# Optimization experiments

Measured on AMD Instinct MI355X. Metric: run time of the kernel, lower is better.

## Reference

```python
import jax, jax.numpy as jnp
import numpy as np

B, S, E, H = 2, 2048, 512, 8
HD = E // H  # head dim = 64


def setup_inputs() -> dict:
    key = jax.random.key(0)
    k1, k2, k3 = jax.random.split(key, 3)
    scale_qkv = (6.0 / (E + 3 * E)) ** 0.5  # xavier-uniform-like scale
    scale_o = (6.0 / (E + E)) ** 0.5
    return {
        "X": jax.random.normal(k1, (B, S, E), dtype=jnp.float32),
        "Wqkv": jax.random.uniform(k2, (E, 3 * E), jnp.float32, -scale_qkv, scale_qkv),
        "bqkv": jnp.zeros((3 * E,), jnp.float32),
        "Wo": jax.random.uniform(k3, (E, E), jnp.float32, -scale_o, scale_o),
        "bo": jnp.zeros((E,), jnp.float32),
    }


def reference(X, Wqkv, bqkv, Wo, bo):
    b, s, e = X.shape
    # qkv projection: [B,S,3E] -> [B,S,H,3*HD] -> [B,H,S,3*HD]
    qkv = X @ Wqkv + bqkv
    qkv = qkv.reshape(b, s, H, 3 * HD).transpose(0, 2, 1, 3)
    q, k, v = jnp.array_split(qkv, 3, axis=-1)  # each [B,H,S,HD]
    # naive scaled dot-product attention (full score matrix, per source)
    attn_logits = jnp.einsum("bhqd,bhkd->bhqk", q, k) / jnp.sqrt(jnp.float32(HD))
    attention = jax.nn.softmax(attn_logits, axis=-1)  # [B,H,S,S]
    values = jnp.einsum("bhqk,bhkd->bhqd", attention, v)
    values = values.transpose(0, 2, 1, 3).reshape(b, s, e)
    o = values @ Wo + bo
    return (o, attention)
```

## Files before the change

### kernel.cpp

```cpp
#include <hip/hip_runtime.h>

typedef unsigned short u16;
typedef u16 u16x2 __attribute__((ext_vector_type(2)));
typedef u16 u16x4 __attribute__((ext_vector_type(4)));
typedef u16 u16x8 __attribute__((ext_vector_type(8)));
typedef __bf16 bf16x8 __attribute__((ext_vector_type(8)));
typedef float f32x4 __attribute__((ext_vector_type(4)));
typedef float f32x2 __attribute__((ext_vector_type(2)));

#define MFMA16(A, B, C) __builtin_amdgcn_mfma_f32_16x16x32_bf16(A, B, C, 0, 0, 0)

#define SB 2
#define SS 2048
#define SE 512
#define SH 8
#define SHD 64

__device__ __forceinline__ u16 f2b(float f) {
  union { float f; unsigned u; } v;
  v.f = f;
  unsigned r = v.u + 0x7FFFu + ((v.u >> 16) & 1u);
  return (u16)(r >> 16);
}

__device__ __forceinline__ bf16x8 as_bf16x8(u16x8 v) {
  return __builtin_bit_cast(bf16x8, v);
}

__global__ __launch_bounds__(256)
void convx_kernel(const float* __restrict__ X, u16* __restrict__ Xb)
{
  const int i = (blockIdx.x * 256 + threadIdx.x) * 4;
  const float4 v = *(const float4*)&X[i];
  u16x4 o;
  o[0] = f2b(v.x); o[1] = f2b(v.y); o[2] = f2b(v.z); o[3] = f2b(v.w);
  *(u16x4*)&Xb[i] = o;
}

__global__ __launch_bounds__(256)
void wtrans_kernel(const float* __restrict__ in, u16* __restrict__ out, int N)
{
  __shared__ float t[32][33];
  const int tid = threadIdx.x;
  const int r = tid >> 3, c4 = (tid & 7) * 4;
  const int k0 = blockIdx.y * 32, n0 = blockIdx.x * 32;
  const float4 v = *(const float4*)&in[(size_t)(k0 + r) * N + n0 + c4];
  t[r][c4 + 0] = v.x; t[r][c4 + 1] = v.y; t[r][c4 + 2] = v.z; t[r][c4 + 3] = v.w;
  __syncthreads();
  u16x4 o;
  o[0] = f2b(t[c4 + 0][r]);
  o[1] = f2b(t[c4 + 1][r]);
  o[2] = f2b(t[c4 + 2][r]);
  o[3] = f2b(t[c4 + 3][r]);
  *(u16x4*)&out[(n0 + r) * 512 + k0 + c4] = o;
}

template <int MODE>
__global__ __launch_bounds__(256, 2)
void gemm_kernel(const u16* __restrict__ A, const u16* __restrict__ Bt,
                 const float* __restrict__ bias,
                 u16* __restrict__ Q, u16* __restrict__ K, u16* __restrict__ Vt,
                 float* __restrict__ Out)
{
  __shared__ __align__(16) u16 As[128 * 40];
  __shared__ __align__(16) u16 Bs[128 * 40];
  const int tid  = threadIdx.x;
  const int lane = tid & 63, wave = tid >> 6, quad = lane >> 4, l16 = lane & 15;
  const int m0 = blockIdx.y * 128, n0 = blockIdx.x * 128;
  const int wr = (wave >> 1) * 64, wc = (wave & 1) * 64;
  const int sr = tid >> 2, sc = (tid & 3) * 8;

  const f32x4 z4 = {0.f, 0.f, 0.f, 0.f};
  f32x4 acc[4][4];
#pragma unroll
  for (int i = 0; i < 4; i++)
#pragma unroll
    for (int j = 0; j < 4; j++) acc[i][j] = z4;

  for (int k0 = 0; k0 < 512; k0 += 32) {
    const u16x8 a0 = *(const u16x8*)&A[(m0 + sr) * 512 + k0 + sc];
    const u16x8 a1 = *(const u16x8*)&A[(m0 + 64 + sr) * 512 + k0 + sc];
    const u16x8 b0 = *(const u16x8*)&Bt[(n0 + sr) * 512 + k0 + sc];
    const u16x8 b1 = *(const u16x8*)&Bt[(n0 + 64 + sr) * 512 + k0 + sc];
    __syncthreads();
    *(u16x8*)&As[sr * 40 + sc]        = a0;
    *(u16x8*)&As[(64 + sr) * 40 + sc] = a1;
    *(u16x8*)&Bs[sr * 40 + sc]        = b0;
    *(u16x8*)&Bs[(64 + sr) * 40 + sc] = b1;
    __syncthreads();
    bf16x8 af[4], bf[4];
#pragma unroll
    for (int i = 0; i < 4; i++) {
      af[i] = as_bf16x8(*(const u16x8*)&As[(wr + i * 16 + l16) * 40 + quad * 8]);
      bf[i] = as_bf16x8(*(const u16x8*)&Bs[(wc + i * 16 + l16) * 40 + quad * 8]);
    }
#pragma unroll
    for (int i = 0; i < 4; i++)
#pragma unroll
      for (int j = 0; j < 4; j++) acc[i][j] = MFMA16(af[i], bf[j], acc[i][j]);
  }

#pragma unroll
  for (int tm = 0; tm < 4; tm++) {
#pragma unroll
    for (int tn = 0; tn < 4; tn++) {
#pragma unroll
      for (int r = 0; r < 4; r++) {
        const int gm = m0 + wr + tm * 16 + quad * 4 + r;
        const int gn = n0 + wc + tn * 16 + l16;
        const float v = acc[tm][tn][r] + bias[gn];
        if (MODE == 0) {
          const int bb = gm >> 11, s = gm & 2047;
          const int hh = gn / 192, j = gn - hh * 192;
          const int bh = bb * SH + hh;
          if (j < 64)
            Q[(bh * SS + s) * SHD + j] = f2b(v * 0.125f);
          else if (j < 128)
            K[(bh * SS + s) * SHD + (j - 64)] = f2b(v);
          else
            Vt[(bh * SHD + (j - 128)) * SS + s] = f2b(v);
        } else {
          Out[gm * 512 + gn] = v;
        }
      }
    }
  }
}

#define PSTR 264
#define PWAVE (16 * PSTR)

__global__ __launch_bounds__(512, 4)
void attn_kernel(const u16* __restrict__ Q, const u16* __restrict__ K,
                 const u16* __restrict__ Vt, u16* __restrict__ values,
                 float* __restrict__ attn)
{
  __shared__ __align__(16) u16 p_lds[8 * PWAVE];
  __shared__ float srm[8][16];
  __shared__ float srl[8][16];

  const int tid  = threadIdx.x;
  const int lane = tid & 63, wave = tid >> 6, quad = lane >> 4, l16 = lane & 15;
  const int q0 = blockIdx.x * 16;
  const int h = blockIdx.y, b = blockIdx.z, bh = b * SH + h;

  const u16* Qb = Q + (size_t)bh * SS * SHD;
  const u16* Kb = K + (size_t)bh * SS * SHD;
  const u16* Vb = Vt + (size_t)bh * SHD * SS;

  const bf16x8 aq0 = as_bf16x8(*(const u16x8*)&Qb[(q0 + l16) * SHD + quad * 8]);
  const bf16x8 aq1 = as_bf16x8(*(const u16x8*)&Qb[(q0 + l16) * SHD + 32 + quad * 8]);

  f32x4 acc[16];
#pragma unroll
  for (int ct = 0; ct < 16; ct++) {
    const int kb = wave * 256 + ct * 16;
    bf16x8 bk0 = as_bf16x8(*(const u16x8*)&Kb[(kb + l16) * SHD + quad * 8]);
    bf16x8 bk1 = as_bf16x8(*(const u16x8*)&Kb[(kb + l16) * SHD + 32 + quad * 8]);
    f32x4 c = {0.f, 0.f, 0.f, 0.f};
    c = MFMA16(aq0, bk0, c);
    c = MFMA16(aq1, bk1, c);
    acc[ct] = c;
  }

  float mw[4], lw[4];
#pragma unroll
  for (int r = 0; r < 4; r++) {
    float m = acc[0][r];
#pragma unroll
    for (int ct = 1; ct < 16; ct++) m = fmaxf(m, acc[ct][r]);
#pragma unroll
    for (int off = 1; off < 16; off <<= 1) m = fmaxf(m, __shfl_xor(m, off));
    mw[r] = m;
  }
#pragma unroll
  for (int r = 0; r < 4; r++) {
    float s = 0.f;
#pragma unroll
    for (int ct = 0; ct < 16; ct++) {
      const float p = __expf(acc[ct][r] - mw[r]);
      acc[ct][r] = p;
      s += p;
    }
#pragma unroll
    for (int off = 1; off < 16; off <<= 1) s += __shfl_xor(s, off);
    lw[r] = s;
  }
  if (l16 == 0) {
#pragma unroll
    for (int r = 0; r < 4; r++) {
      srm[wave][quad * 4 + r] = mw[r];
      srl[wave][quad * 4 + r] = lw[r];
    }
  }
  __syncthreads();

  float scale[4];
#pragma unroll
  for (int r = 0; r < 4; r++) {
    const int row = quad * 4 + r;
    float mg = srm[0][row];
#pragma unroll
    for (int w = 1; w < 8; w++) mg = fmaxf(mg, srm[w][row]);
    float lg = 0.f;
#pragma unroll
    for (int w = 0; w < 8; w++) lg += srl[w][row] * __expf(srm[w][row] - mg);
    scale[r] = __expf(mw[r] - mg) / lg;
  }

  float* attn_b = attn + ((size_t)bh * SS + q0) * SS;
  u16* pl = &p_lds[wave * PWAVE];
#pragma unroll
  for (int ct = 0; ct < 16; ct++) {
    const int col = wave * 256 + ct * 16 + l16;
#pragma unroll
    for (int r = 0; r < 4; r++) {
      const float p = acc[ct][r] * scale[r];
      __builtin_nontemporal_store(p, &attn_b[(quad * 4 + r) * SS + col]);
      pl[(quad * 4 + r) * PSTR + ct * 16 + l16] = f2b(p);
    }
  }

  f32x4 oacc[4];
#pragma unroll
  for (int nt = 0; nt < 4; nt++) oacc[nt] = (f32x4){0.f, 0.f, 0.f, 0.f};
#pragma unroll
  for (int kc = 0; kc < 8; kc++) {
    bf16x8 pa = as_bf16x8(*(const u16x8*)&pl[l16 * PSTR + kc * 32 + quad * 8]);
    const int sb = wave * 256 + kc * 32 + quad * 8;
#pragma unroll
    for (int nt = 0; nt < 4; nt++) {
      bf16x8 vb = as_bf16x8(*(const u16x8*)&Vb[(nt * 16 + l16) * SS + sb]);
      oacc[nt] = MFMA16(pa, vb, oacc[nt]);
    }
  }

  float* op = (float*)pl;
#pragma unroll
  for (int nt = 0; nt < 4; nt++)
#pragma unroll
    for (int r = 0; r < 4; r++)
      op[(quad * 4 + r) * 64 + nt * 16 + l16] = oacc[nt][r];
  __syncthreads();

  const int q = tid >> 5, d0 = (tid & 31) * 2;
  f32x2 s2 = {0.f, 0.f};
#pragma unroll
  for (int w = 0; w < 8; w++) {
    const float* opw = (const float*)&p_lds[w * PWAVE];
    s2 += *(const f32x2*)&opw[q * 64 + d0];
  }
  u16x2 o2;
  o2[0] = f2b(s2[0]);
  o2[1] = f2b(s2[1]);
  *(u16x2*)&values[((size_t)(b * SS + q0 + q) * SH + h) * SHD + d0] = o2;
}

extern "C" void kernel_launch(void* const* d_in, const int* in_sizes, int n_in,
                              void* d_out, int out_size, void* d_ws, size_t ws_size,
                              hipStream_t stream) {
  const float* X    = (const float*)d_in[0];
  const float* Wqkv = (const float*)d_in[1];
  const float* bqkv = (const float*)d_in[2];
  const float* Wo   = (const float*)d_in[3];
  const float* bo   = (const float*)d_in[4];

  float* o_out    = (float*)d_out;
  float* attn_out = o_out + SB * SS * SE;

  const size_t QKV_ELEMS = (size_t)SB * SH * SS * SHD;
  u16* Q      = (u16*)d_ws;
  u16* K      = Q + QKV_ELEMS;
  u16* Vt     = K + QKV_ELEMS;
  u16* values = Vt + QKV_ELEMS;
  u16* Xb     = values;
  u16* WqkvT  = (u16*)attn_out;
  u16* WoT    = Q;

  convx_kernel<<<dim3(2048), 256, 0, stream>>>(X, Xb);
  wtrans_kernel<<<dim3(48, 16), 256, 0, stream>>>(Wqkv, WqkvT, 1536);

  gemm_kernel<0><<<dim3(12, 32), 256, 0, stream>>>(Xb, WqkvT, bqkv, Q, K, Vt, nullptr);
  attn_kernel<<<dim3(128, 8, 2), 512, 0, stream>>>(Q, K, Vt, values, attn_out);
  wtrans_kernel<<<dim3(16, 16), 256, 0, stream>>>(Wo, WoT, 512);
  gemm_kernel<1><<<dim3(4, 32), 256, 0, stream>>>(values, WoT, bo,
                                                  nullptr, nullptr, nullptr, o_out);
}
```

Measured before the change: 425.7 us.

## Merge prep kernels, double-buffer V loads, defer attention-matrix stores

Folds the X bf16 conversion and the Wqkv transpose into one launch to save a kernel launch. In the attention kernel, V fragments are double-buffered in registers so the next chunk's global loads are issued before the current MFMAs. The large nontemporal stores of the attention probabilities move to the end of the kernel so they overlap with or follow the PV compute instead of stalling it. The cost is higher register pressure from keeping acc live longer plus the extra vbuf registers, which could lower occupancy.

```diff
diff --git a/kernel.cpp b/kernel.cpp
--- a/kernel.cpp
+++ b/kernel.cpp
@@ -28,13 +28,31 @@
 }
 
 __global__ __launch_bounds__(256)
-void convx_kernel(const float* __restrict__ X, u16* __restrict__ Xb)
+void prep_kernel(const float* __restrict__ X, u16* __restrict__ Xb,
+                 const float* __restrict__ Wqkv, u16* __restrict__ WqkvT)
 {
-  const int i = (blockIdx.x * 256 + threadIdx.x) * 4;
-  const float4 v = *(const float4*)&X[i];
-  u16x4 o;
-  o[0] = f2b(v.x); o[1] = f2b(v.y); o[2] = f2b(v.z); o[3] = f2b(v.w);
-  *(u16x4*)&Xb[i] = o;
+  __shared__ float t[32][33];
+  const int tid = threadIdx.x;
+  if (blockIdx.x < 2048) {
+    const int i = (blockIdx.x * 256 + tid) * 4;
+    const float4 v = *(const float4*)&X[i];
+    u16x4 o;
+    o[0] = f2b(v.x); o[1] = f2b(v.y); o[2] = f2b(v.z); o[3] = f2b(v.w);
+    *(u16x4*)&Xb[i] = o;
+  } else {
+    const int bx = blockIdx.x - 2048;
+    const int n0 = (bx % 48) * 32, k0 = (bx / 48) * 32;
+    const int r = tid >> 3, c4 = (tid & 7) * 4;
+    const float4 v = *(const float4*)&Wqkv[(size_t)(k0 + r) * 1536 + n0 + c4];
+    t[r][c4 + 0] = v.x; t[r][c4 + 1] = v.y; t[r][c4 + 2] = v.z; t[r][c4 + 3] = v.w;
+    __syncthreads();
+    u16x4 o;
+    o[0] = f2b(t[c4 + 0][r]);
+    o[1] = f2b(t[c4 + 1][r]);
+    o[2] = f2b(t[c4 + 2][r]);
+    o[3] = f2b(t[c4 + 3][r]);
+    *(u16x4*)&WqkvT[(n0 + r) * 512 + k0 + c4] = o;
+  }
 }
 
 __global__ __launch_bounds__(256)
@@ -207,32 +225,41 @@
     for (int w = 0; w < 8; w++) lg += srl[w][row] * __expf(srm[w][row] - mg);
     scale[r] = __expf(mw[r] - mg) / lg;
   }
-
-  float* attn_b = attn + ((size_t)bh * SS + q0) * SS;
+#pragma unroll
+  for (int ct = 0; ct < 16; ct++)
+#pragma unroll
+    for (int r = 0; r < 4; r++) acc[ct][r] *= scale[r];
+
   u16* pl = &p_lds[wave * PWAVE];
 #pragma unroll
-  for (int ct = 0; ct < 16; ct++) {
-    const int col = wave * 256 + ct * 16 + l16;
-#pragma unroll
-    for (int r = 0; r < 4; r++) {
-      const float p = acc[ct][r] * scale[r];
-      __builtin_nontemporal_store(p, &attn_b[(quad * 4 + r) * SS + col]);
-      pl[(quad * 4 + r) * PSTR + ct * 16 + l16] = f2b(p);
-    }
-  }
+  for (int ct = 0; ct < 16; ct++)
+#pragma unroll
+    for (int r = 0; r < 4; r++)
+      pl[(quad * 4 + r) * PSTR + ct * 16 + l16] = f2b(acc[ct][r]);
 
   f32x4 oacc[4];
 #pragma unroll
   for (int nt = 0; nt < 4; nt++) oacc[nt] = (f32x4){0.f, 0.f, 0.f, 0.f};
+  bf16x8 vbuf[2][4];
+  {
+    const int sb = wave * 256 + quad * 8;
+#pragma unroll
+    for (int nt = 0; nt < 4; nt++)
+      vbuf[0][nt] = as_bf16x8(*(const u16x8*)&Vb[(nt * 16 + l16) * SS + sb]);
+  }
 #pragma unroll
   for (int kc = 0; kc < 8; kc++) {
+    if (kc < 7) {
+      const int sb = wave * 256 + (kc + 1) * 32 + quad * 8;
+#pragma unroll
+      for (int nt = 0; nt < 4; nt++)
+        vbuf[(kc + 1) & 1][nt] =
+            as_bf16x8(*(const u16x8*)&Vb[(nt * 16 + l16) * SS + sb]);
+    }
     bf16x8 pa = as_bf16x8(*(const u16x8*)&pl[l16 * PSTR + kc * 32 + quad * 8]);
-    const int sb = wave * 256 + kc * 32 + quad * 8;
-#pragma unroll
-    for (int nt = 0; nt < 4; nt++) {
-      bf16x8 vb = as_bf16x8(*(const u16x8*)&Vb[(nt * 16 + l16) * SS + sb]);
-      oacc[nt] = MFMA16(pa, vb, oacc[nt]);
-    }
+#pragma unroll
+    for (int nt = 0; nt < 4; nt++)
+      oacc[nt] = MFMA16(pa, vbuf[kc & 1][nt], oacc[nt]);
   }
 
   float* op = (float*)pl;
@@ -254,6 +281,15 @@
   o2[0] = f2b(s2[0]);
   o2[1] = f2b(s2[1]);
   *(u16x2*)&values[((size_t)(b * SS + q0 + q) * SH + h) * SHD + d0] = o2;
+
+  float* attn_b = attn + ((size_t)bh * SS + q0) * SS;
+#pragma unroll
+  for (int ct = 0; ct < 16; ct++) {
+    const int col = wave * 256 + ct * 16 + l16;
+#pragma unroll
+    for (int r = 0; r < 4; r++)
+      __builtin_nontemporal_store(acc[ct][r], &attn_b[(quad * 4 + r) * SS + col]);
+  }
 }
 
 extern "C" void kernel_launch(void* const* d_in, const int* in_sizes, int n_in,
@@ -277,8 +313,7 @@
   u16* WqkvT  = (u16*)attn_out;
   u16* WoT    = Q;
 
-  convx_kernel<<<dim3(2048), 256, 0, stream>>>(X, Xb);
-  wtrans_kernel<<<dim3(48, 16), 256, 0, stream>>>(Wqkv, WqkvT, 1536);
+  prep_kernel<<<dim3(2816), 256, 0, stream>>>(X, Xb, Wqkv, WqkvT);
 
   gemm_kernel<0><<<dim3(12, 32), 256, 0, stream>>>(Xb, WqkvT, bqkv, Q, K, Vt, nullptr);
   attn_kernel<<<dim3(128, 8, 2), 512, 0, stream>>>(Q, K, Vt, values, attn_out);
```

After: 421.3 us. No clear change (-1.0%).
